# Kernel optimization log

Hardware: AMD Instinct MI355X
Metric: run time of the kernel (lower is better)

## Reference

```python
import jax, jax.numpy as jnp
import numpy as np

IMG, P, C, E = 256, 16, 3, 200
N = (IMG // P) ** 2          # 256 patches
NUM_MASKED = int(N * 0.75)   # 192
PATCH_ELEMS = C * P * P      # 768


def setup_inputs() -> dict:
    key = jax.random.key(0)
    ks = jax.random.split(key, 10)
    B = 128
    x = jax.random.normal(ks[0], (B, C, IMG, IMG), dtype=jnp.float32)
    perm = jax.random.permutation(ks[1], N).astype(jnp.int32)
    conv_w = jax.random.normal(ks[2], (E, C, P, P), dtype=jnp.float32) * 0.02
    conv_b = jnp.zeros((E,), dtype=jnp.float32)
    pos_embed = jax.random.normal(ks[3], (1, N, E), dtype=jnp.float32) * 0.02
    mask_token = jnp.zeros((1, E), dtype=jnp.float32)
    W_enc = jax.random.normal(ks[4], (E, E), dtype=jnp.float32) * (1.0 / np.sqrt(E))
    b_enc = jnp.zeros((E,), dtype=jnp.float32)
    W_dec = jax.random.normal(ks[5], (E, PATCH_ELEMS), dtype=jnp.float32) * (1.0 / np.sqrt(E))
    b_dec = jnp.zeros((PATCH_ELEMS,), dtype=jnp.float32)
    return {"x": x, "conv_w": conv_w, "conv_b": conv_b, "pos_embed": pos_embed,
            "mask_token": mask_token, "W_enc": W_enc, "b_enc": b_enc,
            "W_dec": W_dec, "b_dec": b_dec, "perm": perm}


def _patchify(x):
    # [B,C,H,W] -> [B, N, C*P*P], row-major patch order (matches conv stride=P then flatten)
    B = x.shape[0]
    g = IMG // P
    x = x.reshape(B, C, g, P, g, P)           # B C gh P gw P
    x = x.transpose(0, 2, 4, 1, 3, 5)         # B gh gw C P P
    return x.reshape(B, g * g, C * P * P)


def _fold(patches):
    # [B, N, C*P*P] -> [B,C,H,W]; idx iterates rows (i) outer, cols (j) inner
    B = patches.shape[0]
    g = IMG // P
    p = patches.reshape(B, g, g, C, P, P)
    return p.transpose(0, 3, 1, 4, 2, 5).reshape(B, C, IMG, IMG)


def reference(x, conv_w, conv_b, pos_embed, mask_token, W_enc, b_enc, W_dec, b_dec, perm):
    masked_idx = perm[:NUM_MASKED]
    unmasked_idx = perm[NUM_MASKED:]
    # patch embed (Conv2d k=P, stride=P == linear over flattened patches)
    patches = _patchify(x)                                   # [B,N,768]
    w_flat = conv_w.reshape(E, -1)                           # [E, 768]
    emb = jnp.einsum('bnp,ep->bne', patches, w_flat) + conv_b + pos_embed  # [B,N,E]
    visible = emb[:, unmasked_idx, :]                        # [B, N-192, E]
    encoded = jnp.einsum('bne,ef->bnf', visible, W_enc) + b_enc
    B = x.shape[0]
    full = jnp.zeros((B, N, E), dtype=x.dtype)
    full = full.at[:, unmasked_idx, :].set(encoded)
    full = full.at[:, masked_idx, :].set(jnp.broadcast_to(mask_token, (B, NUM_MASKED, E)))
    full = full + pos_embed
    dec = jnp.einsum('bne,ep->bnp', full, W_dec) + b_dec     # [B,N,768]
    img = _fold(dec)                                         # [B,C,H,W]
    return img, masked_idx
```

## Files before the change

kernel.cpp:

```cpp
#include <hip/hip_runtime.h>

typedef __attribute__((ext_vector_type(8))) __bf16 bf16x8;
typedef __attribute__((ext_vector_type(4))) float f32x4;

constexpr int Bsz   = 128;
constexpr int EE    = 200;
constexpr int EP    = 256;
constexpr int KP    = 224;
constexpr int NN    = 256;
constexpr int NMASK = 192;
constexpr int NVIS  = 64;
constexpr int PE    = 768;
constexpr int M1    = Bsz * NVIS;
constexpr int M3    = M1 + NMASK;
constexpr long IMG_ELEMS = (long)Bsz * 3 * 256 * 256;

constexpr int VBLK = 256;
constexpr int ASTR = 776;
constexpr int TSTR = 264;
constexpr int FOFF = 32 * TSTR;

__device__ __forceinline__ f32x4 mfma16(bf16x8 a, bf16x8 b, f32x4 c) {
    return __builtin_amdgcn_mfma_f32_16x16x32_bf16(a, b, c, 0, 0, 0);
}

__global__ __launch_bounds__(256) void k_prep(
    const float* __restrict__ pos, const float* __restrict__ wflat,
    const float* __restrict__ Wenc, const float* __restrict__ Wdec,
    const float* __restrict__ conv_b, const float* __restrict__ b_enc,
    const float* __restrict__ mask_token, const int* __restrict__ perm,
    float* __restrict__ posP, __bf16* __restrict__ W1t,
    __bf16* __restrict__ W2t, __bf16* __restrict__ W3t,
    float* __restrict__ cbp, float* __restrict__ bep,
    __bf16* __restrict__ full, float* __restrict__ out_idx)
{
    int blk = blockIdx.x, t = threadIdx.x;
    if (blk < 256) {
        posP[blk * 256 + t] = (t < EE) ? pos[blk * EE + t] : 0.f;
        return;
    }
    blk -= 256;
    if (blk < 768) {
        int e = blk / 3, k = (blk % 3) * 256 + t;
        W1t[e * 768 + k] = (e < EE) ? (__bf16)wflat[e * 768 + k] : (__bf16)0.f;
        return;
    }
    blk -= 768;
    if (blk < 256) {
        if (t < KP) W2t[blk * KP + t] =
            (blk < EE && t < EE) ? (__bf16)Wenc[t * EE + blk] : (__bf16)0.f;
        return;
    }
    blk -= 256;
    if (blk < 768) {
        if (t < KP) W3t[blk * KP + t] =
            (t < EE) ? (__bf16)Wdec[t * PE + blk] : (__bf16)0.f;
        return;
    }
    blk -= 768;
    if (blk < NMASK) {
        int n = perm[blk];
        full[(M1 + blk) * EP + t] =
            (t < EE) ? (__bf16)(mask_token[t] + pos[n * EE + t]) : (__bf16)0.f;
        return;
    }
    cbp[t] = (t < EE) ? conv_b[t] : 0.f;
    bep[t] = (t < EE) ? b_enc[t] : 0.f;
    if (t < NMASK) out_idx[t] = (float)perm[t];
}

__global__ __launch_bounds__(512) void k_mega(
    const float* __restrict__ x, const __bf16* __restrict__ W1t,
    const __bf16* __restrict__ W2t, const __bf16* __restrict__ W3t,
    const float* __restrict__ cbp, const float* __restrict__ bep,
    const float* __restrict__ posP, const float* __restrict__ bdec,
    const int* __restrict__ perm, const __bf16* __restrict__ fullg,
    float* __restrict__ img, float* __restrict__ dec_masked)
{
    __shared__ __bf16 smem[32 * ASTR];
    __bf16* As    = smem;
    __bf16* vis_t = smem;
    __bf16* ful_t = smem + FOFF;
    __shared__ int nidx[32];

    const int t    = threadIdx.x;
    const int bid  = blockIdx.x;
    const int lane = t & 63, wid = t >> 6;
    const int quad = lane >> 4, lid = lane & 15;

    if (bid >= VBLK) {
        const int mb = bid - VBLK;
        #pragma unroll
        for (int it = 0; it < 2; ++it) {
            int cchunk = t + it * 512;
            int row = cchunk >> 5, col = (cchunk & 31) * 8;
            *(int4*)&ful_t[row * TSTR + col] =
                *(const int4*)&fullg[(M1 + mb * 32 + row) * EP + col];
        }
        __syncthreads();
        f32x4 acc[2][6] = {};
        const int p0w = wid * 96;
        for (int k0 = 0; k0 < KP; k0 += 32) {
            bf16x8 a0 = *(const bf16x8*)&ful_t[lid * TSTR + k0 + quad * 8];
            bf16x8 a1 = *(const bf16x8*)&ful_t[(16 + lid) * TSTR + k0 + quad * 8];
            #pragma unroll
            for (int j = 0; j < 6; ++j) {
                bf16x8 bv = *(const bf16x8*)&W3t[(p0w + j * 16 + lid) * KP + k0 + quad * 8];
                acc[0][j] = mfma16(a0, bv, acc[0][j]);
                acc[1][j] = mfma16(a1, bv, acc[1][j]);
            }
        }
        #pragma unroll
        for (int j = 0; j < 6; ++j) {
            const int p = p0w + j * 16 + lid;
            const float bd = bdec[p];
            #pragma unroll
            for (int i = 0; i < 2; ++i) {
                const int r0 = mb * 32 + i * 16 + quad * 4;
                #pragma unroll
                for (int r = 0; r < 4; ++r)
                    dec_masked[(r0 + r) * PE + p] = acc[i][j][r] + bd;
            }
        }
        return;
    }

    const int m0 = bid * 32;
    if (t < 32) nidx[t] = perm[NMASK + (m0 & 63) + t];

    {
        const int row = t >> 4;
        const int m = m0 + row;
        const int n = perm[NMASK + (m & 63)];
        const int abase = (m >> 6) * 196608 + (n >> 4) * 4096 + (n & 15) * 16;
        #pragma unroll
        for (int it = 0; it < 6; ++it) {
            int k = (t & 15) * 8 + it * 128;
            int c = k >> 8, py = (k >> 4) & 15, px = k & 15;
            const float* ap = x + abase + c * 65536 + py * 256 + px;
            float4 a0 = *(const float4*)ap;
            float4 a1 = *(const float4*)(ap + 4);
            bf16x8 av;
            av[0] = (__bf16)a0.x; av[1] = (__bf16)a0.y; av[2] = (__bf16)a0.z; av[3] = (__bf16)a0.w;
            av[4] = (__bf16)a1.x; av[5] = (__bf16)a1.y; av[6] = (__bf16)a1.z; av[7] = (__bf16)a1.w;
            *(bf16x8*)&As[row * ASTR + k] = av;
        }
    }
    __syncthreads();

    const int e0w = wid * 32;
    f32x4 acc1[2][2] = {};
    for (int k0 = 0; k0 < 768; k0 += 32) {
        bf16x8 a0 = *(const bf16x8*)&As[lid * ASTR + k0 + quad * 8];
        bf16x8 a1 = *(const bf16x8*)&As[(16 + lid) * ASTR + k0 + quad * 8];
        #pragma unroll
        for (int j = 0; j < 2; ++j) {
            bf16x8 bv = *(const bf16x8*)&W1t[(e0w + j * 16 + lid) * 768 + k0 + quad * 8];
            acc1[0][j] = mfma16(a0, bv, acc1[0][j]);
            acc1[1][j] = mfma16(a1, bv, acc1[1][j]);
        }
    }
    __syncthreads();

    #pragma unroll
    for (int i = 0; i < 2; ++i) {
        const int mloc = i * 16 + quad * 4;
        #pragma unroll
        for (int j = 0; j < 2; ++j) {
            const int e = e0w + j * 16 + lid;
            const float cb = cbp[e];
            #pragma unroll
            for (int r = 0; r < 4; ++r) {
                const int ml = mloc + r;
                vis_t[ml * TSTR + e] =
                    (__bf16)(acc1[i][j][r] + cb + posP[nidx[ml] * 256 + e]);
            }
        }
    }
    __syncthreads();

    f32x4 acc2[2][2] = {};
    for (int k0 = 0; k0 < KP; k0 += 32) {
        bf16x8 a0 = *(const bf16x8*)&vis_t[lid * TSTR + k0 + quad * 8];
        bf16x8 a1 = *(const bf16x8*)&vis_t[(16 + lid) * TSTR + k0 + quad * 8];
        #pragma unroll
        for (int j = 0; j < 2; ++j) {
            bf16x8 bv = *(const bf16x8*)&W2t[(e0w + j * 16 + lid) * KP + k0 + quad * 8];
            acc2[0][j] = mfma16(a0, bv, acc2[0][j]);
            acc2[1][j] = mfma16(a1, bv, acc2[1][j]);
        }
    }
    #pragma unroll
    for (int i = 0; i < 2; ++i) {
        const int mloc = i * 16 + quad * 4;
        #pragma unroll
        for (int j = 0; j < 2; ++j) {
            const int e = e0w + j * 16 + lid;
            const float be = bep[e];
            #pragma unroll
            for (int r = 0; r < 4; ++r) {
                const int ml = mloc + r;
                ful_t[ml * TSTR + e] =
                    (__bf16)(acc2[i][j][r] + be + posP[nidx[ml] * 256 + e]);
            }
        }
    }
    __syncthreads();

    f32x4 acc3[2][6] = {};
    const int p0w = wid * 96;
    for (int k0 = 0; k0 < KP; k0 += 32) {
        bf16x8 a0 = *(const bf16x8*)&ful_t[lid * TSTR + k0 + quad * 8];
        bf16x8 a1 = *(const bf16x8*)&ful_t[(16 + lid) * TSTR + k0 + quad * 8];
        #pragma unroll
        for (int j = 0; j < 6; ++j) {
            bf16x8 bv = *(const bf16x8*)&W3t[(p0w + j * 16 + lid) * KP + k0 + quad * 8];
            acc3[0][j] = mfma16(a0, bv, acc3[0][j]);
            acc3[1][j] = mfma16(a1, bv, acc3[1][j]);
        }
    }
    const int bimg = m0 >> 6;
    #pragma unroll
    for (int j = 0; j < 6; ++j) {
        const int p = p0w + j * 16 + lid;
        const int c = p >> 8, py = (p >> 4) & 15, px = p & 15;
        const float bd = bdec[p];
        const long obase = (long)(bimg * 3 + c) * 65536 + py * 256 + px;
        #pragma unroll
        for (int i = 0; i < 2; ++i) {
            const int mloc = i * 16 + quad * 4;
            #pragma unroll
            for (int r = 0; r < 4; ++r) {
                const int n = nidx[mloc + r];
                img[obase + (n >> 4) * 4096 + (n & 15) * 16] = acc3[i][j][r] + bd;
            }
        }
    }
}

__global__ __launch_bounds__(192) void k_foldmask(
    const float* __restrict__ dec_masked, const int* __restrict__ perm,
    float* __restrict__ img)
{
    const int i  = blockIdx.x;
    const int b0 = blockIdx.y * 8;
    const int n  = perm[i];
    const int t  = threadIdx.x;
    float4 v = *(const float4*)&dec_masked[i * PE + t * 4];
    int p = t * 4;
    int c = p >> 8, py = (p >> 4) & 15, px = p & 15;
    const long base = (long)c * 65536 + (n >> 4) * 4096 + (n & 15) * 16 + py * 256 + px;
    #pragma unroll
    for (int bb = 0; bb < 8; ++bb)
        *(float4*)&img[(long)(b0 + bb) * 3 * 65536 + base] = v;
}

extern "C" void kernel_launch(void* const* d_in, const int* in_sizes, int n_in,
                              void* d_out, int out_size, void* d_ws, size_t ws_size,
                              hipStream_t stream)
{
    const float* x          = (const float*)d_in[0];
    const float* conv_w     = (const float*)d_in[1];
    const float* conv_b     = (const float*)d_in[2];
    const float* pos        = (const float*)d_in[3];
    const float* mask_token = (const float*)d_in[4];
    const float* W_enc      = (const float*)d_in[5];
    const float* b_enc      = (const float*)d_in[6];
    const float* W_dec      = (const float*)d_in[7];
    const float* b_dec      = (const float*)d_in[8];
    const int*   perm       = (const int*)d_in[9];
    float* out = (float*)d_out;

    __bf16* visible = (__bf16*)d_ws;
    __bf16* full    = visible + M1 * EP;
    __bf16* W1t     = full + M3 * EP;
    __bf16* W2t     = W1t + 256 * 768;
    __bf16* W3t     = W2t + 256 * KP;
    float*  posP    = (float*)(W3t + 768 * KP);
    float*  cbp     = posP + 256 * 256;
    float*  bep     = cbp + 256;
    float*  decm    = bep + 256;

    k_prep<<<256 + 768 + 256 + 768 + NMASK + 1, 256, 0, stream>>>(
        pos, conv_w, W_enc, W_dec, conv_b, b_enc, mask_token, perm,
        posP, W1t, W2t, W3t, cbp, bep, full, out + IMG_ELEMS);
    k_mega<<<VBLK + NMASK / 32, 512, 0, stream>>>(
        x, W1t, W2t, W3t, cbp, bep, posP, b_dec, perm, full, out, decm);
    k_foldmask<<<dim3(NMASK, Bsz / 8), 192, 0, stream>>>(decm, perm, out);
}
```

Baseline: 235.9 us.

## Compute masked decode rows in prep, merge mask fold into mega kernel, halve row tile

The masked-row decoder GEMM moves into the prep kernel as a scalar FP32 dot product per block, and the mask-fold broadcast writes move into the main kernel as extra blocks, which removes the separate fold kernel launch. Visible blocks now handle 16 rows instead of 32, doubling the block count and halving shared memory per block, with a launch-bounds occupancy hint added. The aim is better occupancy and load balance across CUs and one fewer launch. The cost is that each W3t/W1t weight read is amortized over half as many rows, and the prep kernel now does scalar FMA work that could lengthen it.

```diff
diff --git a/kernel.cpp b/kernel.cpp
--- a/kernel.cpp
+++ b/kernel.cpp
@@ -7,18 +7,16 @@
 constexpr int EE    = 200;
 constexpr int EP    = 256;
 constexpr int KP    = 224;
-constexpr int NN    = 256;
 constexpr int NMASK = 192;
-constexpr int NVIS  = 64;
 constexpr int PE    = 768;
-constexpr int M1    = Bsz * NVIS;
-constexpr int M3    = M1 + NMASK;
+constexpr int M1    = Bsz * 64;
 constexpr long IMG_ELEMS = (long)Bsz * 3 * 256 * 256;
 
-constexpr int VBLK = 256;
-constexpr int ASTR = 776;
-constexpr int TSTR = 264;
-constexpr int FOFF = 32 * TSTR;
+constexpr int VROWS = 16;
+constexpr int VBLK  = M1 / VROWS;
+constexpr int FBLK  = NMASK * 4;
+constexpr int ASTR  = 776;
+constexpr int TSTR  = 264;
 
 __device__ __forceinline__ f32x4 mfma16(bf16x8 a, bf16x8 b, f32x4 c) {
     return __builtin_amdgcn_mfma_f32_16x16x32_bf16(a, b, c, 0, 0, 0);
@@ -28,12 +26,14 @@
     const float* __restrict__ pos, const float* __restrict__ wflat,
     const float* __restrict__ Wenc, const float* __restrict__ Wdec,
     const float* __restrict__ conv_b, const float* __restrict__ b_enc,
-    const float* __restrict__ mask_token, const int* __restrict__ perm,
+    const float* __restrict__ b_dec, const float* __restrict__ mask_token,
+    const int* __restrict__ perm,
     float* __restrict__ posP, __bf16* __restrict__ W1t,
     __bf16* __restrict__ W2t, __bf16* __restrict__ W3t,
     float* __restrict__ cbp, float* __restrict__ bep,
-    __bf16* __restrict__ full, float* __restrict__ out_idx)
+    float* __restrict__ dec_masked, float* __restrict__ out_idx)
 {
+    __shared__ float rowv[256];
     int blk = blockIdx.x, t = threadIdx.x;
     if (blk < 256) {
         posP[blk * 256 + t] = (t < EE) ? pos[blk * EE + t] : 0.f;
@@ -59,9 +59,21 @@
     }
     blk -= 768;
     if (blk < NMASK) {
-        int n = perm[blk];
-        full[(M1 + blk) * EP + t] =
-            (t < EE) ? (__bf16)(mask_token[t] + pos[n * EE + t]) : (__bf16)0.f;
+        const int i = blk;
+        const int n = perm[i];
+        rowv[t] = (t < EE) ? (mask_token[t] + pos[n * EE + t]) : 0.f;
+        __syncthreads();
+        float a0 = b_dec[t], a1 = b_dec[t + 256], a2 = b_dec[t + 512];
+        #pragma unroll 4
+        for (int k = 0; k < EE; ++k) {
+            const float rv = rowv[k];
+            a0 = fmaf(rv, Wdec[k * PE + t], a0);
+            a1 = fmaf(rv, Wdec[k * PE + t + 256], a1);
+            a2 = fmaf(rv, Wdec[k * PE + t + 512], a2);
+        }
+        dec_masked[i * PE + t]       = a0;
+        dec_masked[i * PE + t + 256] = a1;
+        dec_masked[i * PE + t + 512] = a2;
         return;
     }
     cbp[t] = (t < EE) ? conv_b[t] : 0.f;
@@ -69,19 +81,19 @@
     if (t < NMASK) out_idx[t] = (float)perm[t];
 }
 
-__global__ __launch_bounds__(512) void k_mega(
+__global__ __launch_bounds__(512, 4) void k_mega(
     const float* __restrict__ x, const __bf16* __restrict__ W1t,
     const __bf16* __restrict__ W2t, const __bf16* __restrict__ W3t,
     const float* __restrict__ cbp, const float* __restrict__ bep,
     const float* __restrict__ posP, const float* __restrict__ bdec,
-    const int* __restrict__ perm, const __bf16* __restrict__ fullg,
-    float* __restrict__ img, float* __restrict__ dec_masked)
+    const int* __restrict__ perm, const float* __restrict__ dec_masked,
+    float* __restrict__ img)
 {
-    __shared__ __bf16 smem[32 * ASTR];
+    __shared__ __bf16 smem[VROWS * ASTR];
     __bf16* As    = smem;
     __bf16* vis_t = smem;
-    __bf16* ful_t = smem + FOFF;
-    __shared__ int nidx[32];
+    __bf16* ful_t = smem + VROWS * TSTR;
+    __shared__ int nidx[VROWS];
 
     const int t    = threadIdx.x;
     const int bid  = blockIdx.x;
@@ -89,53 +101,38 @@
     const int quad = lane >> 4, lid = lane & 15;
 
     if (bid >= VBLK) {
-        const int mb = bid - VBLK;
-        #pragma unroll
-        for (int it = 0; it < 2; ++it) {
-            int cchunk = t + it * 512;
-            int row = cchunk >> 5, col = (cchunk & 31) * 8;
-            *(int4*)&ful_t[row * TSTR + col] =
-                *(const int4*)&fullg[(M1 + mb * 32 + row) * EP + col];
-        }
-        __syncthreads();
-        f32x4 acc[2][6] = {};
-        const int p0w = wid * 96;
-        for (int k0 = 0; k0 < KP; k0 += 32) {
-            bf16x8 a0 = *(const bf16x8*)&ful_t[lid * TSTR + k0 + quad * 8];
-            bf16x8 a1 = *(const bf16x8*)&ful_t[(16 + lid) * TSTR + k0 + quad * 8];
+        const int fb  = bid - VBLK;
+        const int i   = fb % NMASK;
+        const int grp = fb / NMASK;
+        const int n   = perm[i];
+        if (t < 384) {
+            const int sub = t / 192, f4 = t % 192;
+            float4 v = *(const float4*)&dec_masked[i * PE + f4 * 4];
+            const int p = f4 * 4;
+            const int c = p >> 8, py = (p >> 4) & 15, px = p & 15;
+            const long base = (long)c * 65536 + ((n >> 4) * 16 + py) * 256
+                            + (n & 15) * 16 + px;
+            const int b0 = grp * 32 + sub * 16;
             #pragma unroll
-            for (int j = 0; j < 6; ++j) {
-                bf16x8 bv = *(const bf16x8*)&W3t[(p0w + j * 16 + lid) * KP + k0 + quad * 8];
-                acc[0][j] = mfma16(a0, bv, acc[0][j]);
-                acc[1][j] = mfma16(a1, bv, acc[1][j]);
-            }
-        }
-        #pragma unroll
-        for (int j = 0; j < 6; ++j) {
-            const int p = p0w + j * 16 + lid;
-            const float bd = bdec[p];
-            #pragma unroll
-            for (int i = 0; i < 2; ++i) {
-                const int r0 = mb * 32 + i * 16 + quad * 4;
-                #pragma unroll
-                for (int r = 0; r < 4; ++r)
-                    dec_masked[(r0 + r) * PE + p] = acc[i][j][r] + bd;
-            }
-        }
-        return;
-    }
-
-    const int m0 = bid * 32;
-    if (t < 32) nidx[t] = perm[NMASK + (m0 & 63) + t];
+            for (int bb = 0; bb < 16; ++bb)
+                *(float4*)&img[(long)(b0 + bb) * 3 * 65536 + base] = v;
+        }
+        return;
+    }
+
+    const int m0   = bid * VROWS;
+    const int bimg = m0 >> 6;
+    if (t < VROWS) nidx[t] = perm[NMASK + (m0 & 63) + t];
 
     {
-        const int row = t >> 4;
+        const int row = t >> 5;
+        const int tt  = t & 31;
         const int m = m0 + row;
         const int n = perm[NMASK + (m & 63)];
-        const int abase = (m >> 6) * 196608 + (n >> 4) * 4096 + (n & 15) * 16;
-        #pragma unroll
-        for (int it = 0; it < 6; ++it) {
-            int k = (t & 15) * 8 + it * 128;
+        const int abase = bimg * 196608 + (n >> 4) * 4096 + (n & 15) * 16;
+        #pragma unroll
+        for (int it = 0; it < 3; ++it) {
+            int k = tt * 8 + it * 256;
             int c = k >> 8, py = (k >> 4) & 15, px = k & 15;
             const float* ap = x + abase + c * 65536 + py * 256 + px;
             float4 a0 = *(const float4*)ap;
@@ -149,77 +146,60 @@
     __syncthreads();
 
     const int e0w = wid * 32;
-    f32x4 acc1[2][2] = {};
+    f32x4 acc1[2] = {};
     for (int k0 = 0; k0 < 768; k0 += 32) {
         bf16x8 a0 = *(const bf16x8*)&As[lid * ASTR + k0 + quad * 8];
-        bf16x8 a1 = *(const bf16x8*)&As[(16 + lid) * ASTR + k0 + quad * 8];
         #pragma unroll
         for (int j = 0; j < 2; ++j) {
             bf16x8 bv = *(const bf16x8*)&W1t[(e0w + j * 16 + lid) * 768 + k0 + quad * 8];
-            acc1[0][j] = mfma16(a0, bv, acc1[0][j]);
-            acc1[1][j] = mfma16(a1, bv, acc1[1][j]);
+            acc1[j] = mfma16(a0, bv, acc1[j]);
         }
     }
     __syncthreads();
 
     #pragma unroll
-    for (int i = 0; i < 2; ++i) {
-        const int mloc = i * 16 + quad * 4;
-        #pragma unroll
-        for (int j = 0; j < 2; ++j) {
-            const int e = e0w + j * 16 + lid;
-            const float cb = cbp[e];
-            #pragma unroll
-            for (int r = 0; r < 4; ++r) {
-                const int ml = mloc + r;
-                vis_t[ml * TSTR + e] =
-                    (__bf16)(acc1[i][j][r] + cb + posP[nidx[ml] * 256 + e]);
-            }
-        }
-    }
-    __syncthreads();
-
-    f32x4 acc2[2][2] = {};
+    for (int j = 0; j < 2; ++j) {
+        const int e = e0w + j * 16 + lid;
+        const float cb = cbp[e];
+        #pragma unroll
+        for (int r = 0; r < 4; ++r) {
+            const int ml = quad * 4 + r;
+            vis_t[ml * TSTR + e] = (__bf16)(acc1[j][r] + cb + posP[nidx[ml] * 256 + e]);
+        }
+    }
+    __syncthreads();
+
+    f32x4 acc2[2] = {};
     for (int k0 = 0; k0 < KP; k0 += 32) {
         bf16x8 a0 = *(const bf16x8*)&vis_t[lid * TSTR + k0 + quad * 8];
-        bf16x8 a1 = *(const bf16x8*)&vis_t[(16 + lid) * TSTR + k0 + quad * 8];
         #pragma unroll
         for (int j = 0; j < 2; ++j) {
             bf16x8 bv = *(const bf16x8*)&W2t[(e0w + j * 16 + lid) * KP + k0 + quad * 8];
-            acc2[0][j] = mfma16(a0, bv, acc2[0][j]);
-            acc2[1][j] = mfma16(a1, bv, acc2[1][j]);
+            acc2[j] = mfma16(a0, bv, acc2[j]);
         }
     }
     #pragma unroll
-    for (int i = 0; i < 2; ++i) {
-        const int mloc = i * 16 + quad * 4;
-        #pragma unroll
-        for (int j = 0; j < 2; ++j) {
-            const int e = e0w + j * 16 + lid;
-            const float be = bep[e];
-            #pragma unroll
-            for (int r = 0; r < 4; ++r) {
-                const int ml = mloc + r;
-                ful_t[ml * TSTR + e] =
-                    (__bf16)(acc2[i][j][r] + be + posP[nidx[ml] * 256 + e]);
-            }
-        }
-    }
-    __syncthreads();
-
-    f32x4 acc3[2][6] = {};
+    for (int j = 0; j < 2; ++j) {
+        const int e = e0w + j * 16 + lid;
+        const float be = bep[e];
+        #pragma unroll
+        for (int r = 0; r < 4; ++r) {
+            const int ml = quad * 4 + r;
+            ful_t[ml * TSTR + e] = (__bf16)(acc2[j][r] + be + posP[nidx[ml] * 256 + e]);
+        }
+    }
+    __syncthreads();
+
+    f32x4 acc3[6] = {};
     const int p0w = wid * 96;
     for (int k0 = 0; k0 < KP; k0 += 32) {
         bf16x8 a0 = *(const bf16x8*)&ful_t[lid * TSTR + k0 + quad * 8];
-        bf16x8 a1 = *(const bf16x8*)&ful_t[(16 + lid) * TSTR + k0 + quad * 8];
         #pragma unroll
         for (int j = 0; j < 6; ++j) {
             bf16x8 bv = *(const bf16x8*)&W3t[(p0w + j * 16 + lid) * KP + k0 + quad * 8];
-            acc3[0][j] = mfma16(a0, bv, acc3[0][j]);
-            acc3[1][j] = mfma16(a1, bv, acc3[1][j]);
-        }
-    }
-    const int bimg = m0 >> 6;
+            acc3[j] = mfma16(a0, bv, acc3[j]);
+        }
+    }
     #pragma unroll
     for (int j = 0; j < 6; ++j) {
         const int p = p0w + j * 16 + lid;
@@ -227,32 +207,11 @@
         const float bd = bdec[p];
         const long obase = (long)(bimg * 3 + c) * 65536 + py * 256 + px;
         #pragma unroll
-        for (int i = 0; i < 2; ++i) {
-            const int mloc = i * 16 + quad * 4;
-            #pragma unroll
-            for (int r = 0; r < 4; ++r) {
-                const int n = nidx[mloc + r];
-                img[obase + (n >> 4) * 4096 + (n & 15) * 16] = acc3[i][j][r] + bd;
-            }
-        }
-    }
-}
-
-__global__ __launch_bounds__(192) void k_foldmask(
-    const float* __restrict__ dec_masked, const int* __restrict__ perm,
-    float* __restrict__ img)
-{
-    const int i  = blockIdx.x;
-    const int b0 = blockIdx.y * 8;
-    const int n  = perm[i];
-    const int t  = threadIdx.x;
-    float4 v = *(const float4*)&dec_masked[i * PE + t * 4];
-    int p = t * 4;
-    int c = p >> 8, py = (p >> 4) & 15, px = p & 15;
-    const long base = (long)c * 65536 + (n >> 4) * 4096 + (n & 15) * 16 + py * 256 + px;
-    #pragma unroll
-    for (int bb = 0; bb < 8; ++bb)
-        *(float4*)&img[(long)(b0 + bb) * 3 * 65536 + base] = v;
+        for (int r = 0; r < 4; ++r) {
+            const int n = nidx[quad * 4 + r];
+            img[obase + (n >> 4) * 4096 + (n & 15) * 16] = acc3[j][r] + bd;
+        }
+    }
 }
 
 extern "C" void kernel_launch(void* const* d_in, const int* in_sizes, int n_in,
@@ -273,7 +232,7 @@
 
     __bf16* visible = (__bf16*)d_ws;
     __bf16* full    = visible + M1 * EP;
-    __bf16* W1t     = full + M3 * EP;
+    __bf16* W1t     = full + (M1 + NMASK) * EP;
     __bf16* W2t     = W1t + 256 * 768;
     __bf16* W3t     = W2t + 256 * KP;
     float*  posP    = (float*)(W3t + 768 * KP);
@@ -282,9 +241,8 @@
     float*  decm    = bep + 256;
 
     k_prep<<<256 + 768 + 256 + 768 + NMASK + 1, 256, 0, stream>>>(
-        pos, conv_w, W_enc, W_dec, conv_b, b_enc, mask_token, perm,
-        posP, W1t, W2t, W3t, cbp, bep, full, out + IMG_ELEMS);
-    k_mega<<<VBLK + NMASK / 32, 512, 0, stream>>>(
-        x, W1t, W2t, W3t, cbp, bep, posP, b_dec, perm, full, out, decm);
-    k_foldmask<<<dim3(NMASK, Bsz / 8), 192, 0, stream>>>(decm, perm, out);
-}
+        pos, conv_w, W_enc, W_dec, conv_b, b_enc, b_dec, mask_token, perm,
+        posP, W1t, W2t, W3t, cbp, bep, decm, out + IMG_ELEMS);
+    k_mega<<<VBLK + FBLK, 512, 0, stream>>>(
+        x, W1t, W2t, W3t, cbp, bep, posP, b_dec, perm, decm, out);
+}
```

New measurement: 238.8 us. About the same (+1.3%).
